# Optimization experiments

Measured on AMD Instinct MI355X. Metric: run time of the kernel, lower is better.

The kernel has to match this reference:

```python
import jax, jax.numpy as jnp
import numpy as np

EPS = 1e-5      # BatchNorm1d default eps
K = 4           # branching factor of the ontology tree
HID = 6         # num_hiddens_genotype
LEVEL_SIZES = (64, 16, 4, 1)   # leaves -> root (term_layer_list order)
OFFSETS = (0, 64, 80, 84)      # slices into the stacked [85,...] term params


def setup_inputs() -> dict:
    key = jax.random.key(0)
    ks = jax.random.split(key, 8)
    B, G, GD, NT, NL = 4096, 4096, 24, 85, 64
    f32 = jnp.float32
    return {
        "x": jax.random.normal(ks[0], (B, G), f32),
        "gene_W": jax.random.normal(ks[1], (NL, GD, G), f32) * (1.0 / np.sqrt(G)),
        "gene_b": jnp.zeros((NL, GD), f32),
        "term_W": jax.random.normal(ks[2], (NT, HID, GD), f32) * (1.0 / np.sqrt(GD)),
        "term_b": jnp.zeros((NT, HID), f32),
        "bn_gamma": jnp.ones((NT, HID), f32),
        "bn_beta": jnp.zeros((NT, HID), f32),
        "aux1_W": jax.random.normal(ks[3], (NT, 1, HID), f32) * 0.1,
        "aux1_b": jnp.zeros((NT, 1), f32),
        "aux2_W": jax.random.normal(ks[4], (NT, 1, 1), f32) * 0.1,
        "aux2_b": jnp.zeros((NT, 1), f32),
        "final_W": jax.random.normal(ks[5], (HID, HID), f32) * (1.0 / np.sqrt(HID)),
        "final_b": jnp.zeros((HID,), f32),
        "fbn_gamma": jnp.ones((HID,), f32),
        "fbn_beta": jnp.zeros((HID,), f32),
        "faux_W": jax.random.normal(ks[6], (1, HID), f32) * 0.1,
        "faux_b": jnp.zeros((1,), f32),
        "fout_W": jax.random.normal(ks[7], (1, 1), f32) * 0.1,
        "fout_b": jnp.zeros((1,), f32),
    }


def _bn(z, g, b):
    # training-mode BatchNorm1d: batch mean / biased variance over axis 0
    mu = jnp.mean(z, axis=0, keepdims=True)
    var = jnp.mean((z - mu) ** 2, axis=0, keepdims=True)
    return (z - mu) * jax.lax.rsqrt(var + EPS) * g + b


def _forward(x, gene_W, gene_b, term_W, term_b, bn_gamma, bn_beta,
             aux1_W, aux1_b, aux2_W, aux2_b, final_W, final_b,
             fbn_gamma, fbn_beta, faux_W, faux_b, fout_W, fout_b):
    B = x.shape[0]
    # direct_gene_layers for all 64 leaf terms, batched: [B, 64, 24]
    h_in = jnp.einsum('bg,tkg->btk', x, gene_W) + gene_b
    aux_outs = []
    h = None
    for n, o in zip(LEVEL_SIZES, OFFSETS):  # leaves -> root (DAG topo order)
        if h is not None:
            # concat the K=4 children hidden states of each term: [B,n,K*HID]
            h_in = h.reshape(B, n, K * HID)
        # per-term Linear + tanh + BatchNorm, batched over the n terms
        z = jnp.tanh(jnp.einsum('bti,thi->bth', h_in, term_W[o:o + n]) + term_b[o:o + n])
        h = _bn(z, bn_gamma[o:o + n], bn_beta[o:o + n])  # [B, n, HID]
        # aux head: Linear(HID->1) -> tanh -> Linear(1->1)
        a1 = jnp.tanh(jnp.einsum('bth,toh->bto', h, aux1_W[o:o + n]) + aux1_b[o:o + n])
        a2 = a1 * aux2_W[o:o + n, 0] + aux2_b[o:o + n]   # [B, n, 1]
        aux_outs.append(a2[..., 0])
    root = h[:, 0, :]                                    # [B, HID]
    f = jnp.tanh(root @ final_W.T + final_b)
    mu = jnp.mean(f, axis=0)
    var = jnp.mean((f - mu) ** 2, axis=0)
    f = (f - mu) * jax.lax.rsqrt(var + EPS) * fbn_gamma + fbn_beta
    fa = jnp.tanh(f @ faux_W.T + faux_b)                 # [B, 1]
    pred = jax.nn.sigmoid(fa * fout_W[0, 0] + fout_b)    # [B, 1]
    # aux_out_map flattened in topo order, with 'final' prediction last: [B, 86]
    return jnp.concatenate(aux_outs + [pred], axis=1)


def reference(x, gene_W, gene_b, term_W, term_b, bn_gamma, bn_beta,
              aux1_W, aux1_b, aux2_W, aux2_b, final_W, final_b,
              fbn_gamma, fbn_beta, faux_W, faux_b, fout_W, fout_b):
    return _forward(x, gene_W, gene_b, term_W, term_b, bn_gamma, bn_beta,
                    aux1_W, aux1_b, aux2_W, aux2_b, final_W, final_b,
                    fbn_gamma, fbn_beta, faux_W, faux_b, fout_W, fout_b)
```

## Files before the change

kernel.cpp:

```cpp
#include <hip/hip_runtime.h>
#include <stdint.h>
#include <math.h>

#define EPSV   1e-5f
#define BATCH  4096
#define GDIM   4096
#define NF0    384
#define NSPLIT 8

typedef __attribute__((ext_vector_type(8))) short bf16x8;
typedef __attribute__((ext_vector_type(4))) float f32x4;
typedef __attribute__((ext_vector_type(2))) float f32x2;
typedef __attribute__((ext_vector_type(4))) uint32_t u32x4;

__device__ __forceinline__ uint32_t pkbf(float x, float y) {
    uint32_t a = __float_as_uint(x) + 0x8000u;
    uint32_t b = __float_as_uint(y) + 0x8000u;
    return __builtin_amdgcn_perm(b, a, 0x07060302u);
}
__device__ __forceinline__ uint16_t f2bf(float f) {
    return (uint16_t)((__float_as_uint(f) + 0x8000u) >> 16);
}
__device__ __forceinline__ float blo(uint32_t v) {
    union { uint32_t u; float f; } x; x.u = v << 16; return x.f;
}
__device__ __forceinline__ float bhi(uint32_t v) {
    union { uint32_t u; float f; } x; x.u = v & 0xffff0000u; return x.f;
}
__device__ __forceinline__ void glds16(const uint16_t* g, short* l) {
    __builtin_amdgcn_global_load_lds(
        (const __attribute__((address_space(1))) void*)g,
        (__attribute__((address_space(3))) void*)l, 16, 0, 0);
}

__global__ __launch_bounds__(256) void prep_kernel(
    const float* __restrict__ gene_W,
    const float* __restrict__ term_W, const float* __restrict__ term_b,
    const float* __restrict__ gene_b,
    uint16_t* __restrict__ m0, float* __restrict__ stats)
{
    const int tid = threadIdx.x;
    if (blockIdx.x == 0) {
        for (int j = tid; j < 1040; j += 256) stats[j] = 0.f;
        for (int f = tid; f < NF0; f += 256) {
            const int t = f / 6, h = f - t * 6;
            float b = term_b[f];
#pragma unroll
            for (int i = 0; i < 24; ++i)
                b += term_W[t * 144 + h * 24 + i] * gene_b[t * 24 + i];
            stats[1040 + f] = b;
        }
    }
    __shared__ float Wl[144];
    const int bid = blockIdx.x;
    const int t = bid >> 4;
    const int g = ((bid & 15) << 8) + tid;
    if (tid < 144) Wl[tid] = term_W[t * 144 + tid];
    __syncthreads();
    float gw[24];
#pragma unroll
    for (int i = 0; i < 24; ++i)
        gw[i] = gene_W[((size_t)t * 24 + i) * GDIM + g];
#pragma unroll
    for (int h = 0; h < 6; ++h) {
        float s = 0.f;
#pragma unroll
        for (int i = 0; i < 24; ++i) s += Wl[h * 24 + i] * gw[i];
        m0[((size_t)(t * 6 + h)) * GDIM + g] = f2bf(s);
    }
}

__global__ __launch_bounds__(256) void gemm_glds(
    const float* __restrict__ A32, const uint16_t* __restrict__ Bw,
    uint16_t* __restrict__ P, int KC)
{
    const int N = NF0, K = GDIM;
    __shared__ short sA[128 * 32];
    __shared__ short sB[2][128 * 32];
    const int tid  = threadIdx.x;
    const int m0   = blockIdx.y * 128, n0 = blockIdx.x * 128;
    const int kbase = blockIdx.z * KC;
    uint16_t* Cp = P + (size_t)blockIdx.z * ((size_t)BATCH * NF0);
    const int wave = tid >> 6, lane = tid & 63;
    const int wm   = (wave & 1) << 6, wn = (wave >> 1) << 6;
    const int lm   = lane & 15, quad = lane >> 4;

    f32x4 acc[4][4];
#pragma unroll
    for (int i = 0; i < 4; ++i)
#pragma unroll
        for (int j = 0; j < 4; ++j) acc[i][j] = (f32x4){0.f, 0.f, 0.f, 0.f};

    const int r0  = tid >> 2;
    const int c0e = (tid & 3) << 3;
    const float*    gA = A32 + (size_t)(m0 + r0) * K + kbase + c0e;
    const uint16_t* gB = Bw  + (size_t)(n0 + r0) * K + kbase + c0e;
    short* la0 = &sA[tid * 8];
    short* la1 = &sA[2048 + tid * 8];
    const size_t rowskip = (size_t)64 * K;

    glds16(gB,            &sB[0][tid * 8]);
    glds16(gB + rowskip,  &sB[0][2048 + tid * 8]);
    f32x4 a0 = *(const f32x4*)(gA);
    f32x4 a1 = *(const f32x4*)(gA + 4);
    f32x4 a2 = *(const f32x4*)(gA + rowskip);
    f32x4 a3 = *(const f32x4*)(gA + rowskip + 4);

    int cur = 0;
    for (int k0 = 0; k0 < KC - 32; k0 += 32) {
        const int kn = k0 + 32;
        glds16(gB + kn,           &sB[cur ^ 1][tid * 8]);
        glds16(gB + rowskip + kn, &sB[cur ^ 1][2048 + tid * 8]);
        f32x4 n0v = *(const f32x4*)(gA + kn);
        f32x4 n1v = *(const f32x4*)(gA + kn + 4);
        f32x4 n2v = *(const f32x4*)(gA + rowskip + kn);
        f32x4 n3v = *(const f32x4*)(gA + rowskip + kn + 4);
        asm volatile("s_waitcnt vmcnt(6)" ::: "memory");
        u32x4 pa0 = (u32x4){pkbf(a0[0],a0[1]), pkbf(a0[2],a0[3]),
                            pkbf(a1[0],a1[1]), pkbf(a1[2],a1[3])};
        u32x4 pa1 = (u32x4){pkbf(a2[0],a2[1]), pkbf(a2[2],a2[3]),
                            pkbf(a3[0],a3[1]), pkbf(a3[2],a3[3])};
        *(u32x4*)la0 = pa0;
        *(u32x4*)la1 = pa1;
        asm volatile("s_waitcnt lgkmcnt(0)" ::: "memory");
        __builtin_amdgcn_s_barrier();
        bf16x8 af[4], bfr[4];
#pragma unroll
        for (int m = 0; m < 4; ++m)
            af[m]  = *(const bf16x8*)&sA[(wm + m * 16 + lm) * 32 + quad * 8];
#pragma unroll
        for (int n = 0; n < 4; ++n)
            bfr[n] = *(const bf16x8*)&sB[cur][(wn + n * 16 + lm) * 32 + quad * 8];
#pragma unroll
        for (int m = 0; m < 4; ++m)
#pragma unroll
            for (int n = 0; n < 4; ++n)
                acc[m][n] = __builtin_amdgcn_mfma_f32_16x16x32_bf16(
                    af[m], bfr[n], acc[m][n], 0, 0, 0);
        __builtin_amdgcn_s_barrier();
        a0 = n0v; a1 = n1v; a2 = n2v; a3 = n3v;
        cur ^= 1;
    }
    asm volatile("s_waitcnt vmcnt(0)" ::: "memory");
    {
        u32x4 pa0 = (u32x4){pkbf(a0[0],a0[1]), pkbf(a0[2],a0[3]),
                            pkbf(a1[0],a1[1]), pkbf(a1[2],a1[3])};
        u32x4 pa1 = (u32x4){pkbf(a2[0],a2[1]), pkbf(a2[2],a2[3]),
                            pkbf(a3[0],a3[1]), pkbf(a3[2],a3[3])};
        *(u32x4*)la0 = pa0;
        *(u32x4*)la1 = pa1;
    }
    asm volatile("s_waitcnt lgkmcnt(0)" ::: "memory");
    __builtin_amdgcn_s_barrier();
    {
        bf16x8 af[4], bfr[4];
#pragma unroll
        for (int m = 0; m < 4; ++m)
            af[m]  = *(const bf16x8*)&sA[(wm + m * 16 + lm) * 32 + quad * 8];
#pragma unroll
        for (int n = 0; n < 4; ++n)
            bfr[n] = *(const bf16x8*)&sB[cur][(wn + n * 16 + lm) * 32 + quad * 8];
#pragma unroll
        for (int m = 0; m < 4; ++m)
#pragma unroll
            for (int n = 0; n < 4; ++n)
                acc[m][n] = __builtin_amdgcn_mfma_f32_16x16x32_bf16(
                    af[m], bfr[n], acc[m][n], 0, 0, 0);
    }
#pragma unroll
    for (int n = 0; n < 4; ++n) {
        const int col = n0 + wn + n * 16 + lm;
#pragma unroll
        for (int m = 0; m < 4; ++m) {
            const int row = m0 + wm + m * 16 + (quad << 2);
            uint16_t* cp = Cp + (size_t)row * N + col;
#pragma unroll
            for (int r = 0; r < 4; ++r) cp[(size_t)r * N] = f2bf(acc[m][n][r]);
        }
    }
}

__global__ __launch_bounds__(256) void lzero_kernel(
    const uint16_t* __restrict__ P, const float* __restrict__ bias0,
    float* __restrict__ z0, float* __restrict__ st0)
{
    __shared__ float red[4 * 768];
    const int tid  = threadIdx.x;
    const int lane = tid & 63, wave = tid >> 6;
    const uint32_t* P32 = (const uint32_t*)P;

    const f32x2 b0 = ((const f32x2*)bias0)[lane];
    const f32x2 b1 = ((const f32x2*)(bias0 + 128))[lane];
    const f32x2 b2 = ((const f32x2*)(bias0 + 256))[lane];

    float s[6], q[6];
#pragma unroll
    for (int k = 0; k < 6; ++k) { s[k] = 0.f; q[k] = 0.f; }

    const int rbase = blockIdx.x * 8 + wave * 2;
    for (int rl = 0; rl < 2; ++rl) {
        const int r = rbase + rl;
        float a0 = b0[0], a1 = b0[1], a2 = b1[0], a3 = b1[1], a4 = b2[0], a5 = b2[1];
        const uint32_t* pr = P32 + (size_t)r * 192 + lane;
#pragma unroll
        for (int z = 0; z < NSPLIT; ++z) {
            const uint32_t* p = pr + (size_t)z * ((size_t)BATCH * 192);
            uint32_t u0 = p[0], u1 = p[64], u2 = p[128];
            a0 += blo(u0); a1 += bhi(u0);
            a2 += blo(u1); a3 += bhi(u1);
            a4 += blo(u2); a5 += bhi(u2);
        }
        float z0v = tanhf(a0), z1v = tanhf(a1), z2v = tanhf(a2);
        float z3v = tanhf(a3), z4v = tanhf(a4), z5v = tanhf(a5);
        f32x2* zr = (f32x2*)(z0 + (size_t)r * NF0);
        zr[lane]       = (f32x2){z0v, z1v};
        zr[64 + lane]  = (f32x2){z2v, z3v};
        zr[128 + lane] = (f32x2){z4v, z5v};
        s[0] += z0v; q[0] += z0v * z0v;
        s[1] += z1v; q[1] += z1v * z1v;
        s[2] += z2v; q[2] += z2v * z2v;
        s[3] += z3v; q[3] += z3v * z3v;
        s[4] += z4v; q[4] += z4v * z4v;
        s[5] += z5v; q[5] += z5v * z5v;
    }
    float* rw = &red[wave * 768 + lane * 12];
#pragma unroll
    for (int k = 0; k < 6; ++k) { rw[k] = s[k]; rw[6 + k] = q[k]; }
    __syncthreads();
    for (int idx = tid; idx < 768; idx += 256) {
        float v = red[idx] + red[768 + idx] + red[1536 + idx] + red[2304 + idx];
        const int l = idx / 12, k = idx - l * 12;
        const int k6 = k % 6;
        const int f = (k6 >> 1) * 128 + 2 * l + (k6 & 1);
        atomicAdd(&st0[(k >= 6 ? NF0 : 0) + f], v);
    }
}

template <int N, int ROWS, int OFF, int PREV_OFF>
__global__ __launch_bounds__(256) void level_kernel(
    const float* __restrict__ in, float* __restrict__ z_out,
    const float* __restrict__ stats_prev, float* __restrict__ stats_out,
    const float* __restrict__ term_W, const float* __restrict__ term_b,
    const float* __restrict__ bn_gamma, const float* __restrict__ bn_beta,
    const float* __restrict__ aux1_W, const float* __restrict__ aux1_b,
    const float* __restrict__ aux2_W, const float* __restrict__ aux2_b,
    float* __restrict__ out)
{
    constexpr int IN_W  = 24 * N;
    constexpr int NFv   = 6 * N;
    constexpr int NG    = 256 / N;
    constexpr int ITERS = (ROWS * N) / 256;
    constexpr int NPREV = 4 * N;

    __shared__ float Wl[144 * N];
    __shared__ float tbl[6 * N];
    __shared__ float aA[IN_W];
    __shared__ float aC[IN_W];
    __shared__ float a1wL[6 * NPREV];
    __shared__ float a1bL[NPREV], a2wL[NPREV], a2bL[NPREV];
    __shared__ float ps[NG * NFv], pq[NG * NFv];

    const int tid = threadIdx.x;
    for (int idx = tid; idx < 144 * N; idx += 256) {
        int t = idx / 144, fh = idx - t * 144;
        Wl[fh * N + t] = term_W[(OFF + t) * 144 + fh];
    }
    for (int idx = tid; idx < 6 * N; idx += 256) {
        int t = idx / 6, h = idx - t * 6;
        tbl[h * N + t] = term_b[(OFF + t) * 6 + h];
    }
    {
        const float invB = 1.0f / BATCH;
        for (int j = tid; j < IN_W; j += 256) {
            float s = stats_prev[j], q = stats_prev[IN_W + j];
            float mu = s * invB;
            float var = q * invB - mu * mu;
            float rstd = rsqrtf(var + EPSV);
            float a = rstd * bn_gamma[PREV_OFF * 6 + j];
            int t = j / 24, i = j - t * 24;
            aA[i * N + t] = a;
            aC[i * N + t] = bn_beta[PREV_OFF * 6 + j] - mu * a;
        }
        for (int idx = tid; idx < 6 * NPREV; idx += 256) {
            int t = idx / 6, h = idx - t * 6;
            a1wL[h * NPREV + t] = aux1_W[(PREV_OFF + t) * 6 + h];
        }
        for (int t = tid; t < NPREV; t += 256) {
            a1bL[t] = aux1_b[PREV_OFF + t];
            a2wL[t] = aux2_W[PREV_OFF + t];
            a2bL[t] = aux2_b[PREV_OFF + t];
        }
    }
    __syncthreads();

    const int term = tid & (N - 1);
    const int grp  = tid / N;
    float s6[6], q6[6];
#pragma unroll
    for (int h = 0; h < 6; ++h) { s6[h] = 0.f; q6[h] = 0.f; }

    for (int it = 0; it < ITERS; ++it) {
        const int r = blockIdx.x * ROWS + it * NG + grp;
        const float* inrow = in + (size_t)r * IN_W + term * 24;
        float hv[24];
#pragma unroll
        for (int i4 = 0; i4 < 6; ++i4) {
            f32x4 v = *(const f32x4*)(inrow + 4 * i4);
            hv[4*i4+0] = v[0]; hv[4*i4+1] = v[1];
            hv[4*i4+2] = v[2]; hv[4*i4+3] = v[3];
        }
#pragma unroll
        for (int i = 0; i < 24; ++i)
            hv[i] = hv[i] * aA[i * N + term] + aC[i * N + term];
#pragma unroll
        for (int s = 0; s < 4; ++s) {
            const int tp = term * 4 + s;
            float acc = a1bL[tp];
#pragma unroll
            for (int h2 = 0; h2 < 6; ++h2) acc += hv[s * 6 + h2] * a1wL[h2 * NPREV + tp];
            float a1 = tanhf(acc);
            out[(size_t)r * 86 + PREV_OFF + tp] = a1 * a2wL[tp] + a2bL[tp];
        }
        float za[6];
#pragma unroll
        for (int h = 0; h < 6; ++h) za[h] = tbl[h * N + term];
#pragma unroll
        for (int i = 0; i < 24; ++i) {
            const float x = hv[i];
#pragma unroll
            for (int h = 0; h < 6; ++h) za[h] += x * Wl[(h * 24 + i) * N + term];
        }
        float* zr = z_out + (size_t)r * NFv + term * 6;
#pragma unroll
        for (int h = 0; h < 6; ++h) {
            float z = tanhf(za[h]);
            zr[h] = z;
            s6[h] += z;
            q6[h] += z * z;
        }
    }
#pragma unroll
    for (int h = 0; h < 6; ++h) {
        ps[grp * NFv + term * 6 + h] = s6[h];
        pq[grp * NFv + term * 6 + h] = q6[h];
    }
    __syncthreads();
    for (int f = tid; f < NFv; f += 256) {
        float s = 0.f, q = 0.f;
        for (int g2 = 0; g2 < NG; ++g2) { s += ps[g2 * NFv + f]; q += pq[g2 * NFv + f]; }
        atomicAdd(&stats_out[f], s);
        atomicAdd(&stats_out[NFv + f], q);
    }
}

__global__ __launch_bounds__(1024) void final_fused(
    const float* __restrict__ z3, const float* __restrict__ st3,
    const float* __restrict__ bn_gamma, const float* __restrict__ bn_beta,
    const float* __restrict__ aux1_W, const float* __restrict__ aux1_b,
    const float* __restrict__ aux2_W, const float* __restrict__ aux2_b,
    const float* __restrict__ final_W, const float* __restrict__ final_b,
    const float* __restrict__ fbn_gamma, const float* __restrict__ fbn_beta,
    const float* __restrict__ faux_W, const float* __restrict__ faux_b,
    const float* __restrict__ fout_W, const float* __restrict__ fout_b,
    float* __restrict__ out)
{
    __shared__ float wred[16][12];
    __shared__ float fstat[12];
    const int tid = threadIdx.x;
    const float invB = 1.0f / BATCH;
    float a[6], c[6], fw[36], fbv[6];
#pragma unroll
    for (int j = 0; j < 6; ++j) {
        float s = st3[j], q = st3[6 + j];
        float mu = s * invB, var = q * invB - mu * mu;
        float rstd = rsqrtf(var + EPSV);
        a[j] = rstd * bn_gamma[84 * 6 + j];
        c[j] = bn_beta[84 * 6 + j] - mu * a[j];
        fbv[j] = final_b[j];
    }
#pragma unroll
    for (int j = 0; j < 36; ++j) fw[j] = final_W[j];

    float s6[6], q6[6];
#pragma unroll
    for (int j = 0; j < 6; ++j) { s6[j] = 0.f; q6[j] = 0.f; }

    for (int i = 0; i < 4; ++i) {
        const int r = i * 1024 + tid;
        float h[6];
#pragma unroll
        for (int j = 0; j < 6; ++j) h[j] = z3[(size_t)r * 6 + j] * a[j] + c[j];
        float acc = aux1_b[84];
#pragma unroll
        for (int j = 0; j < 6; ++j) acc += h[j] * aux1_W[84 * 6 + j];
        out[(size_t)r * 86 + 84] = tanhf(acc) * aux2_W[84] + aux2_b[84];
#pragma unroll
        for (int j = 0; j < 6; ++j) {
            float s = fbv[j];
#pragma unroll
            for (int k = 0; k < 6; ++k) s += h[k] * fw[j * 6 + k];
            float f = tanhf(s);
            s6[j] += f; q6[j] += f * f;
        }
    }
#pragma unroll
    for (int off = 32; off >= 1; off >>= 1) {
#pragma unroll
        for (int j = 0; j < 6; ++j) {
            s6[j] += __shfl_xor(s6[j], off, 64);
            q6[j] += __shfl_xor(q6[j], off, 64);
        }
    }
    const int wv = tid >> 6, ln = tid & 63;
    if (ln == 0) {
#pragma unroll
        for (int j = 0; j < 6; ++j) { wred[wv][j] = s6[j]; wred[wv][6 + j] = q6[j]; }
    }
    __syncthreads();
    if (tid < 12) {
        float s = 0.f;
#pragma unroll
        for (int w = 0; w < 16; ++w) s += wred[w][tid];
        fstat[tid] = s;
    }
    __syncthreads();
    float av[6], cv[6];
#pragma unroll
    for (int j = 0; j < 6; ++j) {
        float mu = fstat[j] * invB, var = fstat[6 + j] * invB - mu * mu;
        float rstd = rsqrtf(var + EPSV);
        av[j] = rstd * fbn_gamma[j];
        cv[j] = fbn_beta[j] - mu * av[j];
    }
    const float fxb0 = faux_b[0], foW0 = fout_W[0], fob0 = fout_b[0];
    for (int i = 0; i < 4; ++i) {
        const int r = i * 1024 + tid;
        float h[6];
#pragma unroll
        for (int j = 0; j < 6; ++j) h[j] = z3[(size_t)r * 6 + j] * a[j] + c[j];
        float acc2 = fxb0;
#pragma unroll
        for (int j = 0; j < 6; ++j) {
            float s = fbv[j];
#pragma unroll
            for (int k = 0; k < 6; ++k) s += h[k] * fw[j * 6 + k];
            float fn = tanhf(s) * av[j] + cv[j];
            acc2 += fn * faux_W[j];
        }
        float fa  = tanhf(acc2);
        float pre = fa * foW0 + fob0;
        out[(size_t)r * 86 + 85] = 1.0f / (1.0f + expf(-pre));
    }
}

extern "C" void kernel_launch(void* const* d_in, const int* in_sizes, int n_in,
                              void* d_out, int out_size, void* d_ws, size_t ws_size,
                              hipStream_t stream)
{
    const float* x      = (const float*)d_in[0];
    const float* gene_W = (const float*)d_in[1];
    const float* gene_b = (const float*)d_in[2];
    const float* term_W = (const float*)d_in[3];
    const float* term_b = (const float*)d_in[4];
    const float* bn_g   = (const float*)d_in[5];
    const float* bn_b   = (const float*)d_in[6];
    const float* a1W    = (const float*)d_in[7];
    const float* a1b    = (const float*)d_in[8];
    const float* a2W    = (const float*)d_in[9];
    const float* a2b    = (const float*)d_in[10];
    const float* fW     = (const float*)d_in[11];
    const float* fb     = (const float*)d_in[12];
    const float* fbn_g  = (const float*)d_in[13];
    const float* fbn_b  = (const float*)d_in[14];
    const float* fxW    = (const float*)d_in[15];
    const float* fxb    = (const float*)d_in[16];
    const float* foW    = (const float*)d_in[17];
    const float* fob    = (const float*)d_in[18];
    float* out = (float*)d_out;

    const size_t M0B = (size_t)NF0 * GDIM * 2;
    const size_t PB  = (size_t)NSPLIT * BATCH * NF0 * 2;
    const size_t Z0B = (size_t)BATCH * NF0 * 4;

    char* ws = (char*)d_ws;
    uint16_t* m0b  = (uint16_t*)ws;
    uint16_t* pbuf = (uint16_t*)(ws + M0B);
    float*    z0   = (float*)(ws + M0B + PB);
    float*    z1   = (float*)(ws + M0B + PB + Z0B);
    float*    z2   = (float*)(ws + M0B + PB + Z0B + 1572864);
    float*    z3   = (float*)(ws + M0B + PB + Z0B + 1572864 + 393216);
    float*    stats = (float*)(ws + M0B + PB + Z0B + 1572864 + 393216 + 98304);
    float* st0 = stats;
    float* st1 = stats + 768;
    float* st2 = stats + 960;
    float* st3 = stats + 1008;
    float* bias0 = stats + 1040;

    prep_kernel<<<1024, 256, 0, stream>>>(gene_W, term_W, term_b, gene_b,
                                          m0b, stats);
    gemm_glds<<<dim3(3, 32, NSPLIT), 256, 0, stream>>>(x, m0b, pbuf, GDIM / NSPLIT);
    lzero_kernel<<<512, 256, 0, stream>>>(pbuf, bias0, z0, st0);
    level_kernel<16, 16, 64, 0><<<256, 256, 0, stream>>>(
        z0, z1, st0, st1, term_W, term_b, bn_g, bn_b, a1W, a1b, a2W, a2b, out);
    level_kernel<4, 64, 80, 64><<<64, 256, 0, stream>>>(
        z1, z2, st1, st2, term_W, term_b, bn_g, bn_b, a1W, a1b, a2W, a2b, out);
    level_kernel<1, 256, 84, 80><<<16, 256, 0, stream>>>(
        z2, z3, st2, st3, term_W, term_b, bn_g, bn_b, a1W, a1b, a2W, a2b, out);
    final_fused<<<1, 1024, 0, stream>>>(
        z3, st3, bn_g, bn_b, a1W, a1b, a2W, a2b, fW, fb,
        fbn_g, fbn_b, fxW, fxb, foW, fob, out);
}
```

Measured before the change: 257.3 us.

## Split single-block final kernel into two multi-block kernels with atomic stats

The final stage previously ran as one 1024-thread block that made two passes over all 4096 rows and recomputed the 6x6 linear layer and its tanh in the second pass. It is now two kernels of 16 blocks each. The first computes the root aux output and the tanh features, stores them to a workspace buffer, and atomically accumulates BN sums. The second reads those stored features to apply the final BN and output head. This spreads the work across more compute units and avoids recomputing the tanh, at the cost of one extra launch, a small global round-trip, and reliance on the new stats slot being zeroed beforehand.

```diff
diff --git a/kernel.cpp b/kernel.cpp
--- a/kernel.cpp
+++ b/kernel.cpp
@@ -353,104 +353,109 @@
     }
 }
 
-__global__ __launch_bounds__(1024) void final_fused(
+__global__ __launch_bounds__(256) void final_p1(
     const float* __restrict__ z3, const float* __restrict__ st3,
     const float* __restrict__ bn_gamma, const float* __restrict__ bn_beta,
     const float* __restrict__ aux1_W, const float* __restrict__ aux1_b,
     const float* __restrict__ aux2_W, const float* __restrict__ aux2_b,
     const float* __restrict__ final_W, const float* __restrict__ final_b,
+    float* __restrict__ fbuf, float* __restrict__ stf,
+    float* __restrict__ out)
+{
+    __shared__ float wred[4][12];
+    const int tid = threadIdx.x;
+    const int r = blockIdx.x * 256 + tid;
+    const float invB = 1.0f / BATCH;
+    float a[6], c[6];
+#pragma unroll
+    for (int j = 0; j < 6; ++j) {
+        float s = st3[j], q = st3[6 + j];
+        float mu = s * invB, var = q * invB - mu * mu;
+        float rstd = rsqrtf(var + EPSV);
+        a[j] = rstd * bn_gamma[504 + j];
+        c[j] = bn_beta[504 + j] - mu * a[j];
+    }
+    float h[6];
+    {
+        f32x2 z01 = *(const f32x2*)(z3 + (size_t)r * 6);
+        f32x2 z23 = *(const f32x2*)(z3 + (size_t)r * 6 + 2);
+        f32x2 z45 = *(const f32x2*)(z3 + (size_t)r * 6 + 4);
+        h[0] = z01[0] * a[0] + c[0]; h[1] = z01[1] * a[1] + c[1];
+        h[2] = z23[0] * a[2] + c[2]; h[3] = z23[1] * a[3] + c[3];
+        h[4] = z45[0] * a[4] + c[4]; h[5] = z45[1] * a[5] + c[5];
+    }
+    float acc = aux1_b[84];
+#pragma unroll
+    for (int j = 0; j < 6; ++j) acc += h[j] * aux1_W[504 + j];
+    out[(size_t)r * 86 + 84] = tanhf(acc) * aux2_W[84] + aux2_b[84];
+
+    float f[6], s6[6], q6[6];
+#pragma unroll
+    for (int j = 0; j < 6; ++j) {
+        float s = final_b[j];
+#pragma unroll
+        for (int k = 0; k < 6; ++k) s += h[k] * final_W[j * 6 + k];
+        f[j] = tanhf(s);
+        s6[j] = f[j]; q6[j] = f[j] * f[j];
+    }
+    {
+        f32x2* fr = (f32x2*)(fbuf + (size_t)r * 6);
+        fr[0] = (f32x2){f[0], f[1]};
+        fr[1] = (f32x2){f[2], f[3]};
+        fr[2] = (f32x2){f[4], f[5]};
+    }
+#pragma unroll
+    for (int off = 32; off >= 1; off >>= 1) {
+#pragma unroll
+        for (int j = 0; j < 6; ++j) {
+            s6[j] += __shfl_xor(s6[j], off, 64);
+            q6[j] += __shfl_xor(q6[j], off, 64);
+        }
+    }
+    const int wv = tid >> 6, ln = tid & 63;
+    if (ln == 0) {
+#pragma unroll
+        for (int j = 0; j < 6; ++j) { wred[wv][j] = s6[j]; wred[wv][6 + j] = q6[j]; }
+    }
+    __syncthreads();
+    if (tid < 12) {
+        float s = wred[0][tid] + wred[1][tid] + wred[2][tid] + wred[3][tid];
+        atomicAdd(&stf[tid], s);
+    }
+}
+
+__global__ __launch_bounds__(256) void final_p2(
+    const float* __restrict__ fbuf, const float* __restrict__ stf,
     const float* __restrict__ fbn_gamma, const float* __restrict__ fbn_beta,
     const float* __restrict__ faux_W, const float* __restrict__ faux_b,
     const float* __restrict__ fout_W, const float* __restrict__ fout_b,
     float* __restrict__ out)
 {
-    __shared__ float wred[16][12];
-    __shared__ float fstat[12];
     const int tid = threadIdx.x;
+    const int r = blockIdx.x * 256 + tid;
     const float invB = 1.0f / BATCH;
-    float a[6], c[6], fw[36], fbv[6];
+    float av[6], cv[6];
 #pragma unroll
     for (int j = 0; j < 6; ++j) {
-        float s = st3[j], q = st3[6 + j];
-        float mu = s * invB, var = q * invB - mu * mu;
-        float rstd = rsqrtf(var + EPSV);
-        a[j] = rstd * bn_gamma[84 * 6 + j];
-        c[j] = bn_beta[84 * 6 + j] - mu * a[j];
-        fbv[j] = final_b[j];
-    }
-#pragma unroll
-    for (int j = 0; j < 36; ++j) fw[j] = final_W[j];
-
-    float s6[6], q6[6];
-#pragma unroll
-    for (int j = 0; j < 6; ++j) { s6[j] = 0.f; q6[j] = 0.f; }
-
-    for (int i = 0; i < 4; ++i) {
-        const int r = i * 1024 + tid;
-        float h[6];
-#pragma unroll
-        for (int j = 0; j < 6; ++j) h[j] = z3[(size_t)r * 6 + j] * a[j] + c[j];
-        float acc = aux1_b[84];
-#pragma unroll
-        for (int j = 0; j < 6; ++j) acc += h[j] * aux1_W[84 * 6 + j];
-        out[(size_t)r * 86 + 84] = tanhf(acc) * aux2_W[84] + aux2_b[84];
-#pragma unroll
-        for (int j = 0; j < 6; ++j) {
-            float s = fbv[j];
-#pragma unroll
-            for (int k = 0; k < 6; ++k) s += h[k] * fw[j * 6 + k];
-            float f = tanhf(s);
-            s6[j] += f; q6[j] += f * f;
-        }
-    }
-#pragma unroll
-    for (int off = 32; off >= 1; off >>= 1) {
-#pragma unroll
-        for (int j = 0; j < 6; ++j) {
-            s6[j] += __shfl_xor(s6[j], off, 64);
-            q6[j] += __shfl_xor(q6[j], off, 64);
-        }
-    }
-    const int wv = tid >> 6, ln = tid & 63;
-    if (ln == 0) {
-#pragma unroll
-        for (int j = 0; j < 6; ++j) { wred[wv][j] = s6[j]; wred[wv][6 + j] = q6[j]; }
-    }
-    __syncthreads();
-    if (tid < 12) {
-        float s = 0.f;
-#pragma unroll
-        for (int w = 0; w < 16; ++w) s += wred[w][tid];
-        fstat[tid] = s;
-    }
-    __syncthreads();
-    float av[6], cv[6];
-#pragma unroll
-    for (int j = 0; j < 6; ++j) {
-        float mu = fstat[j] * invB, var = fstat[6 + j] * invB - mu * mu;
+        float mu = stf[j] * invB, var = stf[6 + j] * invB - mu * mu;
         float rstd = rsqrtf(var + EPSV);
         av[j] = rstd * fbn_gamma[j];
         cv[j] = fbn_beta[j] - mu * av[j];
     }
-    const float fxb0 = faux_b[0], foW0 = fout_W[0], fob0 = fout_b[0];
-    for (int i = 0; i < 4; ++i) {
-        const int r = i * 1024 + tid;
-        float h[6];
-#pragma unroll
-        for (int j = 0; j < 6; ++j) h[j] = z3[(size_t)r * 6 + j] * a[j] + c[j];
-        float acc2 = fxb0;
-#pragma unroll
-        for (int j = 0; j < 6; ++j) {
-            float s = fbv[j];
-#pragma unroll
-            for (int k = 0; k < 6; ++k) s += h[k] * fw[j * 6 + k];
-            float fn = tanhf(s) * av[j] + cv[j];
-            acc2 += fn * faux_W[j];
-        }
-        float fa  = tanhf(acc2);
-        float pre = fa * foW0 + fob0;
-        out[(size_t)r * 86 + 85] = 1.0f / (1.0f + expf(-pre));
-    }
+    float f[6];
+    {
+        f32x2 f01 = *(const f32x2*)(fbuf + (size_t)r * 6);
+        f32x2 f23 = *(const f32x2*)(fbuf + (size_t)r * 6 + 2);
+        f32x2 f45 = *(const f32x2*)(fbuf + (size_t)r * 6 + 4);
+        f[0] = f01[0]; f[1] = f01[1]; f[2] = f23[0];
+        f[3] = f23[1]; f[4] = f45[0]; f[5] = f45[1];
+    }
+    float acc2 = faux_b[0];
+#pragma unroll
+    for (int j = 0; j < 6; ++j) acc2 += (f[j] * av[j] + cv[j]) * faux_W[j];
+    float fa  = tanhf(acc2);
+    float pre = fa * fout_W[0] + fout_b[0];
+    out[(size_t)r * 86 + 85] = 1.0f / (1.0f + expf(-pre));
 }
 
 extern "C" void kernel_launch(void* const* d_in, const int* in_sizes, int n_in,
@@ -494,7 +499,9 @@
     float* st1 = stats + 768;
     float* st2 = stats + 960;
     float* st3 = stats + 1008;
+    float* stf = stats + 1020;
     float* bias0 = stats + 1040;
+    float* fbuf  = stats + 2048;
 
     prep_kernel<<<1024, 256, 0, stream>>>(gene_W, term_W, term_b, gene_b,
                                           m0b, stats);
@@ -506,7 +513,8 @@
         z1, z2, st1, st2, term_W, term_b, bn_g, bn_b, a1W, a1b, a2W, a2b, out);
     level_kernel<1, 256, 84, 80><<<16, 256, 0, stream>>>(
         z2, z3, st2, st3, term_W, term_b, bn_g, bn_b, a1W, a1b, a2W, a2b, out);
-    final_fused<<<1, 1024, 0, stream>>>(
-        z3, st3, bn_g, bn_b, a1W, a1b, a2W, a2b, fW, fb,
-        fbn_g, fbn_b, fxW, fxb, foW, fob, out);
-}
+    final_p1<<<16, 256, 0, stream>>>(
+        z3, st3, bn_g, bn_b, a1W, a1b, a2W, a2b, fW, fb, fbuf, stf, out);
+    final_p2<<<16, 256, 0, stream>>>(
+        fbuf, stf, fbn_g, fbn_b, fxW, fxb, foW, fob, out);
+}
```

Result: faster. 244.5 us (-5.0%).
